# Optimization experiments

Hardware: AMD Instinct MI355X
Metric: run time of the kernel (lower is better)

Reference implementation:

```python
import jax, jax.numpy as jnp
import numpy as np

B, D, S, F, C, H, OUT = 4, 60, 512, 158, 64, 128, 1
LN_EPS = 1e-5


def setup_inputs() -> dict:
    key = jax.random.key(0)
    ks = jax.random.split(key, 12)
    g = lambda k, shape, s=0.05: jax.random.normal(k, shape, dtype=jnp.float32) * s
    return dict(
        x=jax.random.normal(ks[0], (B, D, S, F), dtype=jnp.float32),
        feature_mask=jax.random.randint(ks[1], (B, D, S), 0, 2).astype(bool),
        wq=g(ks[2], (F, C)), bq=jnp.zeros((C,), jnp.float32),
        wk=g(ks[3], (F, C)), bk=jnp.zeros((C,), jnp.float32),
        wv=g(ks[4], (F, C)), bv=jnp.zeros((C,), jnp.float32),
        ln_g=jnp.ones((F + C,), jnp.float32), ln_b=jnp.zeros((F + C,), jnp.float32),
        w_ih=g(ks[5], (3 * H, F + C)), w_hh=g(ks[6], (3 * H, H)),
        b_ih=jnp.zeros((3 * H,), jnp.float32), b_hh=jnp.zeros((3 * H,), jnp.float32),
        w1=g(ks[7], (H, H // 2)), b1=jnp.zeros((H // 2,), jnp.float32),
        w2=g(ks[8], (H // 2, OUT)), b2=jnp.zeros((OUT,), jnp.float32),
    )


def reference(x, feature_mask, wq, bq, wk, bk, wv, bv, ln_g, ln_b,
              w_ih, w_hh, b_ih, b_hh, w1, b1, w2, b2):
    b, d, s, f = x.shape
    c = wq.shape[1]
    h_dim = w_hh.shape[1]

    # --- market context attention, vectorized over (batch, days) ---
    Q = x @ wq + bq            # (B,D,S,C)
    K = x @ wk + bk
    V = x @ wv + bv
    scores = jnp.einsum('bdsc,bdtc->bdst', Q, K) / jnp.sqrt(jnp.float32(c))
    scores = jnp.where(feature_mask[:, :, None, :], scores, -1e9)  # mask keys
    attn = jax.nn.softmax(scores, axis=-1)
    ctx = jnp.einsum('bdst,bdtc->bdsc', attn, V)       # (B,D,S,C)
    ctx = jnp.where(feature_mask[..., None], ctx, 0.0)  # mask queries
    denom = jnp.maximum(feature_mask.sum(axis=2), 1).astype(x.dtype)  # (B,D)
    market = ctx.sum(axis=2) / denom[..., None]         # (B,D,C)

    # --- concat + layernorm ---
    aug = jnp.concatenate(
        [x, jnp.broadcast_to(market[:, :, None, :], (b, d, s, c))], axis=-1)
    mu = aug.mean(-1, keepdims=True)
    var = aug.var(-1, keepdims=True)
    aug = (aug - mu) / jnp.sqrt(var + LN_EPS) * ln_g + ln_b  # (B,D,S,F+C)

    # --- GRU over days, batch = B*S independent sequences ---
    seq = aug.transpose(1, 0, 2, 3).reshape(d, b * s, f + c)  # (D, N, F+C)
    x_proj = seq @ w_ih.T + b_ih                               # (D, N, 3H)

    def step(h, xp):
        hp = h @ w_hh.T + b_hh
        xr, xz, xn = jnp.split(xp, 3, axis=-1)
        hr, hz, hn = jnp.split(hp, 3, axis=-1)
        r = jax.nn.sigmoid(xr + hr)
        z = jax.nn.sigmoid(xz + hz)
        n = jnp.tanh(xn + r * hn)
        return (1.0 - z) * n + z * h, None

    h0 = jnp.zeros((b * s, h_dim), x.dtype)
    h_last, _ = jax.lax.scan(step, h0, x_proj)  # last-step output
    h_last = h_last.reshape(b, s, h_dim)

    # --- output head (dropout inactive in eval) ---
    hid = jax.nn.relu(h_last @ w1 + b1)
    return hid @ w2 + b2  # (B, S, OUT)
```

## Files before the change

kernel.cpp:

```cpp
#include <hip/hip_runtime.h>
#include <hip/hip_bf16.h>
#include <math.h>

#define BB 4
#define DD 60
#define SS 512
#define FF 158
#define CC 64
#define HH 128
#define FC 222
#define G3 384
#define NN 2048
#define BDN 240

typedef _Float16 f16x8 __attribute__((ext_vector_type(8)));
typedef float f32x4 __attribute__((ext_vector_type(4)));

__device__ __forceinline__ float sigmoidf_(float x){ return 1.0f/(1.0f+__expf(-x)); }
__device__ __forceinline__ float tanh_fast_(float x){
    float e = __expf(2.0f*x);
    return 1.0f - 2.0f/(e + 1.0f);
}

__global__ void prep_kernel(const float* __restrict__ w_ih,
                            const float* __restrict__ wq, const float* __restrict__ wk,
                            const float* __restrict__ wv, const float* __restrict__ w_hh,
                            _Float16* __restrict__ wf16, _Float16* __restrict__ wqkv,
                            _Float16* __restrict__ whh16){
    int idx = blockIdx.x*256 + threadIdx.x;
    if (idx < 384*224){
        int n = idx / 224, k = idx % 224;
        wf16[idx] = (k < FC) ? (_Float16)w_ih[n*FC + k] : (_Float16)0.0f;
    } else if (idx < 384*224 + 192*160){
        int i2 = idx - 384*224;
        int n = i2 / 160, k = i2 % 160;
        float v = 0.0f;
        if (k < FF){
            if (n < 64)       v = wq[k*CC + n];
            else if (n < 128) v = wk[k*CC + (n-64)];
            else              v = wv[k*CC + (n-128)];
        }
        wqkv[i2] = (_Float16)v;
    } else {
        int i3 = idx - (384*224 + 192*160);
        if (i3 < 384*128)
            whh16[i3] = (_Float16)w_hh[i3];
    }
}

__global__ __launch_bounds__(256) void qkv_kernel(const float* __restrict__ x,
                           const _Float16* __restrict__ wqkv,
                           const float* __restrict__ bq, const float* __restrict__ bk,
                           const float* __restrict__ bv,
                           _Float16* __restrict__ Qh, _Float16* __restrict__ Kh,
                           float* __restrict__ V){
    __shared__ _Float16 xa[5][64][40];
    int tid  = threadIdx.x;
    int lane = tid & 63, wv = tid >> 6;
    int col  = lane & 15, quad = lane >> 4;
    int row0 = blockIdx.x * 64;

    f16x8 bfr[3][5];
    #pragma unroll
    for (int nt = 0; nt < 3; ++nt){
        int n = wv*48 + nt*16 + col;
        #pragma unroll
        for (int kq = 0; kq < 5; ++kq)
            bfr[nt][kq] = *(const f16x8*)&wqkv[n*160 + kq*32 + quad*8];
    }

    for (int i = tid; i < 64*160; i += 256){
        int r = i / 160, k = i % 160;
        float v = (k < FF) ? x[(size_t)(row0 + r)*FF + k] : 0.0f;
        xa[k >> 5][r][k & 31] = (_Float16)v;
    }
    __syncthreads();

    float bias[3];
    #pragma unroll
    for (int nt = 0; nt < 3; ++nt){
        int n = wv*48 + nt*16 + col;
        bias[nt] = (n < 64) ? bq[n] : (n < 128 ? bk[n-64] : bv[n-128]);
    }

    #pragma unroll 1
    for (int mt = 0; mt < 4; ++mt){
        f16x8 a[5];
        #pragma unroll
        for (int kq = 0; kq < 5; ++kq)
            a[kq] = *(const f16x8*)&xa[kq][mt*16 + col][quad*8];
        #pragma unroll
        for (int nt = 0; nt < 3; ++nt){
            f32x4 c = {0.0f, 0.0f, 0.0f, 0.0f};
            #pragma unroll
            for (int kq = 0; kq < 5; ++kq)
                c = __builtin_amdgcn_mfma_f32_16x16x32_f16(a[kq], bfr[nt][kq], c, 0, 0, 0);
            int n = wv*48 + nt*16 + col;
            #pragma unroll
            for (int reg = 0; reg < 4; ++reg){
                int row = row0 + mt*16 + quad*4 + reg;
                float val = c[reg] + bias[nt];
                if (n < 64)       Qh[(size_t)row*CC + n]       = (_Float16)val;
                else if (n < 128) Kh[(size_t)row*CC + (n-64)]  = (_Float16)val;
                else              V [(size_t)row*CC + (n-128)] = val;
            }
        }
    }
}

__global__ __launch_bounds__(512) void attn_kernel(const _Float16* __restrict__ Qh,
                                                   const _Float16* __restrict__ Kh,
                                                   const int* __restrict__ mask,
                                                   const float* __restrict__ V,
                                                   float* __restrict__ market){
    __shared__ _Float16 kf[2][512][32];
    __shared__ float w_sh[512];
    __shared__ float mk_lds[512];

    int tid  = threadIdx.x;
    int bd   = blockIdx.x;
    int lane = tid & 63, wv = tid >> 6;
    int col  = lane & 15, quad = lane >> 4;

    const _Float16* qb = Qh + (size_t)(bd*SS)*CC;
    const _Float16* kb = Kh + (size_t)(bd*SS)*CC;

    {
        int t = tid;
        w_sh[t] = 0.0f;
        mk_lds[t] = (mask[bd*SS + t] != 0) ? 1.0f : 0.0f;
    }
    for (int i = tid; i < 4096; i += 512){
        int t = i >> 3, ch = i & 7;
        *(f16x8*)&kf[ch >> 2][t][(ch & 3)*8] = *(const f16x8*)&kb[t*CC + ch*8];
    }

    f16x8 a0[4], a1[4];
    #pragma unroll
    for (int af = 0; af < 4; ++af){
        int row = wv*64 + af*16 + col;
        a0[af] = *(const f16x8*)&qb[row*CC + quad*8];
        a1[af] = *(const f16x8*)&qb[row*CC + 32 + quad*8];
    }
    __syncthreads();

    float lacc[4][4] = {{0,0,0,0},{0,0,0,0},{0,0,0,0},{0,0,0,0}};
    #pragma unroll 2
    for (int kt = 0; kt < 32; ++kt){
        f16x8 b0 = *(const f16x8*)&kf[0][kt*16 + col][quad*8];
        f16x8 b1 = *(const f16x8*)&kf[1][kt*16 + col][quad*8];
        float mkv = mk_lds[kt*16 + col];
        #pragma unroll
        for (int af = 0; af < 4; ++af){
            f32x4 c = {0.0f, 0.0f, 0.0f, 0.0f};
            c = __builtin_amdgcn_mfma_f32_16x16x32_f16(a0[af], b0, c, 0, 0, 0);
            c = __builtin_amdgcn_mfma_f32_16x16x32_f16(a1[af], b1, c, 0, 0, 0);
            #pragma unroll
            for (int reg = 0; reg < 4; ++reg)
                lacc[af][reg] += __expf(c[reg]*0.125f) * mkv;
        }
    }
    float crv[4][4];
    #pragma unroll
    for (int af = 0; af < 4; ++af){
        #pragma unroll
        for (int reg = 0; reg < 4; ++reg){
            float l = lacc[af][reg];
            l += __shfl_xor(l, 1, 64);
            l += __shfl_xor(l, 2, 64);
            l += __shfl_xor(l, 4, 64);
            l += __shfl_xor(l, 8, 64);
            int row = wv*64 + af*16 + quad*4 + reg;
            crv[af][reg] = mk_lds[row] / l;
        }
    }

    #pragma unroll 2
    for (int kt = 0; kt < 32; ++kt){
        f16x8 b0 = *(const f16x8*)&kf[0][kt*16 + col][quad*8];
        f16x8 b1 = *(const f16x8*)&kf[1][kt*16 + col][quad*8];
        float s = 0.0f;
        #pragma unroll
        for (int af = 0; af < 4; ++af){
            f32x4 c = {0.0f, 0.0f, 0.0f, 0.0f};
            c = __builtin_amdgcn_mfma_f32_16x16x32_f16(a0[af], b0, c, 0, 0, 0);
            c = __builtin_amdgcn_mfma_f32_16x16x32_f16(a1[af], b1, c, 0, 0, 0);
            #pragma unroll
            for (int reg = 0; reg < 4; ++reg)
                s = fmaf(__expf(c[reg]*0.125f), crv[af][reg], s);
        }
        s += __shfl_xor(s, 16, 64);
        s += __shfl_xor(s, 32, 64);
        if (quad == 0)
            atomicAdd(&w_sh[kt*16 + col], s);
    }
    __syncthreads();

    float* msum = (float*)kf;
    {
        int c = tid & 63, grp = tid >> 6;
        const float* vb = V + (size_t)(bd*SS)*CC;
        float acc = 0.0f;
        int t0 = grp*64;
        #pragma unroll 4
        for (int t = t0; t < t0 + 64; ++t)
            acc = fmaf(w_sh[t]*mk_lds[t], vb[(size_t)t*CC + c], acc);
        msum[grp*64 + c] = acc;
    }
    __syncthreads();
    if (tid < 64){
        float s = 0.0f;
        #pragma unroll
        for (int g = 0; g < 8; ++g) s += msum[g*64 + tid];
        float cnt = 0.0f;
        #pragma unroll
        for (int j = 0; j < 8; ++j) cnt += mk_lds[tid + 64*j];
        #pragma unroll
        for (int o = 1; o < 64; o <<= 1) cnt += __shfl_xor(cnt, o, 64);
        market[bd*CC + tid] = s / fmaxf(cnt, 1.0f);
    }
}

__global__ __launch_bounds__(512, 2) void xproj_kernel(const float* __restrict__ x,
                             const float* __restrict__ market,
                             const float* __restrict__ ln_g, const float* __restrict__ ln_b,
                             const _Float16* __restrict__ wf16, const float* __restrict__ b_ih,
                             _Float16* __restrict__ XP){
    __shared__ _Float16 aug[7][64][32];
    int tid  = threadIdx.x;
    int lane = tid & 63, wv = tid >> 6;
    int col  = lane & 15, quad = lane >> 4;
    int row0 = blockIdx.x * 64;

    f16x8 bfr[3][7];
    #pragma unroll
    for (int nt = 0; nt < 3; ++nt){
        int n = wv*48 + nt*16 + col;
        #pragma unroll
        for (int kq = 0; kq < 7; ++kq)
            bfr[nt][kq] = *(const f16x8*)&wf16[n*224 + kq*32 + quad*8];
    }

    {
        int wrow = wv*8 + (lane >> 3);
        int g    = lane & 7;
        int row  = row0 + wrow;
        int d = row / NN, n = row % NN;
        int b = n >> 9, s = n & 511;
        const float* xr = &x[((size_t)((b*DD + d)*SS) + s)*FF];
        const float* mr = &market[(b*DD + d)*CC];
        float v[28];
        float sum = 0.0f, sq = 0.0f;
        #pragma unroll
        for (int j = 0; j < 28; ++j){
            int f = g + 8*j;
            float vv = 0.0f;
            if (f < FF) vv = xr[f];
            else if (f < FC) vv = mr[f - FF];
            v[j] = vv;
            sum += vv; sq += vv*vv;
        }
        sum += __shfl_xor(sum,1,64); sq += __shfl_xor(sq,1,64);
        sum += __shfl_xor(sum,2,64); sq += __shfl_xor(sq,2,64);
        sum += __shfl_xor(sum,4,64); sq += __shfl_xor(sq,4,64);
        float mu   = sum * (1.0f/222.0f);
        float var  = sq * (1.0f/222.0f) - mu*mu;
        float rstd = rsqrtf(var + 1e-5f);
        #pragma unroll
        for (int j = 0; j < 28; ++j){
            int f = g + 8*j;
            float val = (f < FC) ? ((v[j]-mu)*rstd*ln_g[f] + ln_b[f]) : 0.0f;
            aug[f>>5][wrow][f&31] = (_Float16)val;
        }
    }
    __syncthreads();

    float bias[3];
    #pragma unroll
    for (int nt = 0; nt < 3; ++nt) bias[nt] = b_ih[wv*48 + nt*16 + col];
    #pragma unroll 1
    for (int mt = 0; mt < 4; ++mt){
        f16x8 a[7];
        #pragma unroll
        for (int kq = 0; kq < 7; ++kq)
            a[kq] = *(const f16x8*)&aug[kq][mt*16 + col][quad*8];
        #pragma unroll
        for (int nt = 0; nt < 3; ++nt){
            f32x4 c = {0.0f, 0.0f, 0.0f, 0.0f};
            #pragma unroll
            for (int kq = 0; kq < 7; ++kq)
                c = __builtin_amdgcn_mfma_f32_16x16x32_f16(a[kq], bfr[nt][kq], c, 0, 0, 0);
            int nn = wv*48 + nt*16 + col;
            #pragma unroll
            for (int reg = 0; reg < 4; ++reg){
                int m = quad*4 + reg;
                XP[(size_t)(row0 + mt*16 + m)*G3 + nn] = (_Float16)(c[reg] + bias[nt]);
            }
        }
    }
}

#define XLOAD(dst, base_) do{                                                   \
    _Pragma("unroll") for (int rg_ = 0; rg_ < 4; ++rg_)                         \
    _Pragma("unroll") for (int g_ = 0; g_ < 3; ++g_)                            \
        dst[rg_][g_] = (base_)[rg_*G3 + g_*HH];                                 \
}while(0)

#define BARRIER_NODRAIN() asm volatile("s_waitcnt lgkmcnt(0)\ns_barrier" ::: "memory")

#define GRU_STEP(PRD, PWR, XC, XPF, DOPF) do{                                   \
    if (DOPF) { XLOAD(XPF, xp_d + 2*DSTR); }                                    \
    f16x8 a_[4];                                                                \
    _Pragma("unroll") for (int kq = 0; kq < 4; ++kq)                            \
        a_[kq] = *(const f16x8*)&hfrag[PRD][kq][col][quad*8];                   \
    f32x4 c0 = {0,0,0,0}, c1 = {0,0,0,0}, c2 = {0,0,0,0};                       \
    _Pragma("unroll") for (int kq = 0; kq < 4; ++kq)                            \
        c0 = __builtin_amdgcn_mfma_f32_16x16x32_f16(a_[kq], bfr[0][kq], c0, 0,0,0); \
    _Pragma("unroll") for (int kq = 0; kq < 4; ++kq)                            \
        c1 = __builtin_amdgcn_mfma_f32_16x16x32_f16(a_[kq], bfr[1][kq], c1, 0,0,0); \
    _Pragma("unroll") for (int kq = 0; kq < 4; ++kq)                            \
        c2 = __builtin_amdgcn_mfma_f32_16x16x32_f16(a_[kq], bfr[2][kq], c2, 0,0,0); \
    _Pragma("unroll") for (int rg = 0; rg < 4; ++rg){                           \
        float r_ = sigmoidf_((float)XC[rg][0] + c0[rg] + bh0);                  \
        float z_ = sigmoidf_((float)XC[rg][1] + c1[rg] + bh1);                  \
        float n_ = tanh_fast_((float)XC[rg][2] + r_*(c2[rg] + bh2));            \
        float h_ = n_ + z_*(hcur[rg] - n_);                                     \
        hcur[rg] = h_;                                                          \
        hfrag[PWR][w >> 1][quad*4 + rg][(w & 1)*16 + col] = (_Float16)h_;       \
    }                                                                           \
    xp_d += DSTR;                                                               \
    BARRIER_NODRAIN();                                                          \
}while(0)

__global__ __launch_bounds__(512) void gru_kernel(const _Float16* __restrict__ XP,
                                                  const _Float16* __restrict__ whh16,
                                                  const float* __restrict__ b_hh,
                                                  const float* __restrict__ w1, const float* __restrict__ b1,
                                                  const float* __restrict__ w2, const float* __restrict__ b2,
                                                  float* __restrict__ out){
    __shared__ _Float16 hfrag[2][4][16][40];
    __shared__ float h_sh[16][132];

    const int tid  = threadIdx.x;
    const int lane = tid & 63, w = tid >> 6;
    const int col  = lane & 15, quad = lane >> 4;
    const int row0 = blockIdx.x * 16;

    for (int i = tid; i < 2*4*16*40; i += 512)
        ((_Float16*)hfrag)[i] = (_Float16)0.0f;

    f16x8 bfr[3][4];
    #pragma unroll
    for (int g = 0; g < 3; ++g){
        #pragma unroll
        for (int kq = 0; kq < 4; ++kq)
            bfr[g][kq] = *(const f16x8*)&whh16[(size_t)(g*HH + w*16 + col)*HH + kq*32 + quad*8];
    }

    const float bh0 = b_hh[0*HH + w*16 + col];
    const float bh1 = b_hh[1*HH + w*16 + col];
    const float bh2 = b_hh[2*HH + w*16 + col];

    const size_t DSTR = (size_t)NN * G3;
    const _Float16* xp_d = XP + (size_t)(row0 + quad*4)*G3 + (w*16 + col);

    _Float16 xA[4][3], xB[4][3], xC[4][3];
    XLOAD(xA, xp_d);
    XLOAD(xB, xp_d + DSTR);

    float hcur[4] = {0.0f, 0.0f, 0.0f, 0.0f};
    __syncthreads();

    #pragma unroll 1
    for (int ch = 0; ch < 10; ++ch){
        const int pf = (ch < 9);
        GRU_STEP(0, 1, xA, xC, 1);
        GRU_STEP(1, 0, xB, xA, 1);
        GRU_STEP(0, 1, xC, xB, 1);
        GRU_STEP(1, 0, xA, xC, 1);
        GRU_STEP(0, 1, xB, xA, pf);
        GRU_STEP(1, 0, xC, xB, pf);
    }

    #pragma unroll
    for (int rg = 0; rg < 4; ++rg)
        h_sh[quad*4 + rg][w*16 + col] = hcur[rg];
    __syncthreads();

    {
        int c2 = tid & 63;
        int rb = tid >> 6;
        #pragma unroll
        for (int rr = 0; rr < 2; ++rr){
            int r = rb + rr*8;
            float acc = 0.0f;
            #pragma unroll 8
            for (int k = 0; k < 128; ++k)
                acc = fmaf(h_sh[r][k], w1[k*64 + c2], acc);
            float hid = fmaxf(acc + b1[c2], 0.0f);
            float o = hid * w2[c2];
            #pragma unroll
            for (int off = 1; off < 64; off <<= 1) o += __shfl_xor(o, off, 64);
            if (c2 == 0) out[row0 + r] = o + b2[0];
        }
    }
}

extern "C" void kernel_launch(void* const* d_in, const int* in_sizes, int n_in,
                              void* d_out, int out_size, void* d_ws, size_t ws_size,
                              hipStream_t stream) {
    const float* x    = (const float*)d_in[0];
    const int*   mask = (const int*)d_in[1];
    const float* wq   = (const float*)d_in[2];
    const float* bq   = (const float*)d_in[3];
    const float* wk   = (const float*)d_in[4];
    const float* bk   = (const float*)d_in[5];
    const float* wv   = (const float*)d_in[6];
    const float* bv   = (const float*)d_in[7];
    const float* ln_g = (const float*)d_in[8];
    const float* ln_b = (const float*)d_in[9];
    const float* w_ih = (const float*)d_in[10];
    const float* w_hh = (const float*)d_in[11];
    const float* b_ih = (const float*)d_in[12];
    const float* b_hh = (const float*)d_in[13];
    const float* w1   = (const float*)d_in[14];
    const float* b1   = (const float*)d_in[15];
    const float* w2   = (const float*)d_in[16];
    const float* b2   = (const float*)d_in[17];

    float* ws = (float*)d_ws;
    _Float16* Qh  = (_Float16*)ws;
    _Float16* Kh  = (_Float16*)(ws + 3932160);
    float*    V   = ws + 7864320;
    _Float16* XP  = (_Float16*)ws;
    float* market = ws + 23592960;
    _Float16* wf16 = (_Float16*)(ws + 23608320);
    _Float16* wqkv = (_Float16*)(ws + 23651328);
    _Float16* whh16= (_Float16*)(ws + 23666688);

    prep_kernel<<<648, 256, 0, stream>>>(w_ih, wq, wk, wv, w_hh, wf16, wqkv, whh16);
    qkv_kernel<<<1920, 256, 0, stream>>>(x, wqkv, bq, bk, bv, Qh, Kh, V);
    attn_kernel<<<240, 512, 0, stream>>>(Qh, Kh, mask, V, market);
    xproj_kernel<<<1920, 512, 0, stream>>>(x, market, ln_g, ln_b, wf16, b_ih, XP);
    gru_kernel<<<128, 512, 0, stream>>>(XP, whh16, b_hh, w1, b1, w2, b2, (float*)d_out);
}
```

Measured before the change: 375.9 us.

## Fold log2(e) into weights, use hardware exp2/rcp, halve GRU block warps

Pre-scales the GRU input and recurrent weights and biases by log2(e) (2·log2(e) for the candidate gate), and folds the attention 1/sqrt(C) and log2(e) factors into Q. This lets every exponential become a raw hardware exp2 and every division a hardware reciprocal, cutting transcendental cost in the attention softmax and the GRU gates. The GRU kernel also drops from 8 to 4 waves per block, with each wave covering 32 hidden columns in two halves, so it issues twice the MFMAs per wave and synchronises fewer waves at each step's barrier. Risks include a small precision loss from fp16 weight scaling and approximate rcp, and less latency hiding inside the serial recurrence.

```diff
diff --git a/kernel.cpp b/kernel.cpp
--- a/kernel.cpp
+++ b/kernel.cpp
@@ -13,14 +13,15 @@
 #define NN 2048
 #define BDN 240
 
+#define L2E  1.44269504f
+#define L2E2 2.88539008f
+#define QSCALE 0.18033688f
+
 typedef _Float16 f16x8 __attribute__((ext_vector_type(8)));
 typedef float f32x4 __attribute__((ext_vector_type(4)));
 
-__device__ __forceinline__ float sigmoidf_(float x){ return 1.0f/(1.0f+__expf(-x)); }
-__device__ __forceinline__ float tanh_fast_(float x){
-    float e = __expf(2.0f*x);
-    return 1.0f - 2.0f/(e + 1.0f);
-}
+__device__ __forceinline__ float exp2_hw(float x){ return __builtin_amdgcn_exp2f(x); }
+__device__ __forceinline__ float rcp_hw(float x){ return __builtin_amdgcn_rcpf(x); }
 
 __global__ void prep_kernel(const float* __restrict__ w_ih,
                             const float* __restrict__ wq, const float* __restrict__ wk,
@@ -30,7 +31,8 @@
     int idx = blockIdx.x*256 + threadIdx.x;
     if (idx < 384*224){
         int n = idx / 224, k = idx % 224;
-        wf16[idx] = (k < FC) ? (_Float16)w_ih[n*FC + k] : (_Float16)0.0f;
+        float sc = (n < 256) ? L2E : L2E2;
+        wf16[idx] = (k < FC) ? (_Float16)(w_ih[n*FC + k] * sc) : (_Float16)0.0f;
     } else if (idx < 384*224 + 192*160){
         int i2 = idx - 384*224;
         int n = i2 / 160, k = i2 % 160;
@@ -43,8 +45,11 @@
         wqkv[i2] = (_Float16)v;
     } else {
         int i3 = idx - (384*224 + 192*160);
-        if (i3 < 384*128)
-            whh16[i3] = (_Float16)w_hh[i3];
+        if (i3 < 384*128){
+            int n = i3 / 128;
+            float sc = (n < 256) ? L2E : L2E2;
+            whh16[i3] = (_Float16)(w_hh[i3] * sc);
+        }
     }
 }
 
@@ -100,7 +105,7 @@
             for (int reg = 0; reg < 4; ++reg){
                 int row = row0 + mt*16 + quad*4 + reg;
                 float val = c[reg] + bias[nt];
-                if (n < 64)       Qh[(size_t)row*CC + n]       = (_Float16)val;
+                if (n < 64)       Qh[(size_t)row*CC + n]       = (_Float16)(val * QSCALE);
                 else if (n < 128) Kh[(size_t)row*CC + (n-64)]  = (_Float16)val;
                 else              V [(size_t)row*CC + (n-128)] = val;
             }
@@ -157,7 +162,7 @@
             c = __builtin_amdgcn_mfma_f32_16x16x32_f16(a1[af], b1, c, 0, 0, 0);
             #pragma unroll
             for (int reg = 0; reg < 4; ++reg)
-                lacc[af][reg] += __expf(c[reg]*0.125f) * mkv;
+                lacc[af][reg] += exp2_hw(c[reg]) * mkv;
         }
     }
     float crv[4][4];
@@ -171,7 +176,7 @@
             l += __shfl_xor(l, 4, 64);
             l += __shfl_xor(l, 8, 64);
             int row = wv*64 + af*16 + quad*4 + reg;
-            crv[af][reg] = mk_lds[row] / l;
+            crv[af][reg] = mk_lds[row] * rcp_hw(l);
         }
     }
 
@@ -187,7 +192,7 @@
             c = __builtin_amdgcn_mfma_f32_16x16x32_f16(a1[af], b1, c, 0, 0, 0);
             #pragma unroll
             for (int reg = 0; reg < 4; ++reg)
-                s = fmaf(__expf(c[reg]*0.125f), crv[af][reg], s);
+                s = fmaf(exp2_hw(c[reg]), crv[af][reg], s);
         }
         s += __shfl_xor(s, 16, 64);
         s += __shfl_xor(s, 32, 64);
@@ -217,7 +222,7 @@
         for (int j = 0; j < 8; ++j) cnt += mk_lds[tid + 64*j];
         #pragma unroll
         for (int o = 1; o < 64; o <<= 1) cnt += __shfl_xor(cnt, o, 64);
-        market[bd*CC + tid] = s / fmaxf(cnt, 1.0f);
+        market[bd*CC + tid] = s * rcp_hw(fmaxf(cnt, 1.0f));
     }
 }
 
@@ -277,7 +282,10 @@
 
     float bias[3];
     #pragma unroll
-    for (int nt = 0; nt < 3; ++nt) bias[nt] = b_ih[wv*48 + nt*16 + col];
+    for (int nt = 0; nt < 3; ++nt){
+        int n = wv*48 + nt*16 + col;
+        bias[nt] = b_ih[n] * ((n < 256) ? L2E : L2E2);
+    }
     #pragma unroll 1
     for (int mt = 0; mt < 4; ++mt){
         f16x8 a[7];
@@ -301,9 +309,10 @@
 }
 
 #define XLOAD(dst, base_) do{                                                   \
+    _Pragma("unroll") for (int hf_ = 0; hf_ < 2; ++hf_)                         \
     _Pragma("unroll") for (int rg_ = 0; rg_ < 4; ++rg_)                         \
     _Pragma("unroll") for (int g_ = 0; g_ < 3; ++g_)                            \
-        dst[rg_][g_] = (base_)[rg_*G3 + g_*HH];                                 \
+        dst[hf_][rg_][g_] = (base_)[rg_*G3 + g_*HH + hf_*16];                   \
 }while(0)
 
 #define BARRIER_NODRAIN() asm volatile("s_waitcnt lgkmcnt(0)\ns_barrier" ::: "memory")
@@ -313,31 +322,34 @@
     f16x8 a_[4];                                                                \
     _Pragma("unroll") for (int kq = 0; kq < 4; ++kq)                            \
         a_[kq] = *(const f16x8*)&hfrag[PRD][kq][col][quad*8];                   \
-    f32x4 c0 = {0,0,0,0}, c1 = {0,0,0,0}, c2 = {0,0,0,0};                       \
-    _Pragma("unroll") for (int kq = 0; kq < 4; ++kq)                            \
-        c0 = __builtin_amdgcn_mfma_f32_16x16x32_f16(a_[kq], bfr[0][kq], c0, 0,0,0); \
-    _Pragma("unroll") for (int kq = 0; kq < 4; ++kq)                            \
-        c1 = __builtin_amdgcn_mfma_f32_16x16x32_f16(a_[kq], bfr[1][kq], c1, 0,0,0); \
-    _Pragma("unroll") for (int kq = 0; kq < 4; ++kq)                            \
-        c2 = __builtin_amdgcn_mfma_f32_16x16x32_f16(a_[kq], bfr[2][kq], c2, 0,0,0); \
+    f32x4 c_[3][2];                                                             \
+    _Pragma("unroll") for (int g = 0; g < 3; ++g)                               \
+    _Pragma("unroll") for (int hf = 0; hf < 2; ++hf){                           \
+        f32x4 acc = {0.0f, 0.0f, 0.0f, 0.0f};                                   \
+        _Pragma("unroll") for (int kq = 0; kq < 4; ++kq)                        \
+            acc = __builtin_amdgcn_mfma_f32_16x16x32_f16(a_[kq], bfr[g][hf][kq], acc, 0,0,0); \
+        c_[g][hf] = acc;                                                        \
+    }                                                                           \
+    _Pragma("unroll") for (int hf = 0; hf < 2; ++hf)                            \
     _Pragma("unroll") for (int rg = 0; rg < 4; ++rg){                           \
-        float r_ = sigmoidf_((float)XC[rg][0] + c0[rg] + bh0);                  \
-        float z_ = sigmoidf_((float)XC[rg][1] + c1[rg] + bh1);                  \
-        float n_ = tanh_fast_((float)XC[rg][2] + r_*(c2[rg] + bh2));            \
-        float h_ = n_ + z_*(hcur[rg] - n_);                                     \
-        hcur[rg] = h_;                                                          \
-        hfrag[PWR][w >> 1][quad*4 + rg][(w & 1)*16 + col] = (_Float16)h_;       \
+        float r_ = rcp_hw(1.0f + exp2_hw(-((float)XC[hf][rg][0] + c_[0][hf][rg] + bh[0][hf]))); \
+        float z_ = rcp_hw(1.0f + exp2_hw(-((float)XC[hf][rg][1] + c_[1][hf][rg] + bh[1][hf]))); \
+        float e_ = exp2_hw((float)XC[hf][rg][2] + r_*(c_[2][hf][rg] + bh[2][hf])); \
+        float n_ = 1.0f - 2.0f*rcp_hw(e_ + 1.0f);                               \
+        float h_ = n_ + z_*(hcur[hf][rg] - n_);                                 \
+        hcur[hf][rg] = h_;                                                      \
+        hfrag[PWR][w][quad*4 + rg][hf*16 + col] = (_Float16)h_;                 \
     }                                                                           \
     xp_d += DSTR;                                                               \
     BARRIER_NODRAIN();                                                          \
 }while(0)
 
-__global__ __launch_bounds__(512) void gru_kernel(const _Float16* __restrict__ XP,
-                                                  const _Float16* __restrict__ whh16,
-                                                  const float* __restrict__ b_hh,
-                                                  const float* __restrict__ w1, const float* __restrict__ b1,
-                                                  const float* __restrict__ w2, const float* __restrict__ b2,
-                                                  float* __restrict__ out){
+__global__ __launch_bounds__(256, 1) void gru_kernel(const _Float16* __restrict__ XP,
+                                                     const _Float16* __restrict__ whh16,
+                                                     const float* __restrict__ b_hh,
+                                                     const float* __restrict__ w1, const float* __restrict__ b1,
+                                                     const float* __restrict__ w2, const float* __restrict__ b2,
+                                                     float* __restrict__ out){
     __shared__ _Float16 hfrag[2][4][16][40];
     __shared__ float h_sh[16][132];
 
@@ -346,29 +358,35 @@
     const int col  = lane & 15, quad = lane >> 4;
     const int row0 = blockIdx.x * 16;
 
-    for (int i = tid; i < 2*4*16*40; i += 512)
+    for (int i = tid; i < 2*4*16*40; i += 256)
         ((_Float16*)hfrag)[i] = (_Float16)0.0f;
 
-    f16x8 bfr[3][4];
-    #pragma unroll
-    for (int g = 0; g < 3; ++g){
+    f16x8 bfr[3][2][4];
+    #pragma unroll
+    for (int g = 0; g < 3; ++g)
+    #pragma unroll
+    for (int hf = 0; hf < 2; ++hf){
+        int n = g*HH + w*32 + hf*16 + col;
         #pragma unroll
         for (int kq = 0; kq < 4; ++kq)
-            bfr[g][kq] = *(const f16x8*)&whh16[(size_t)(g*HH + w*16 + col)*HH + kq*32 + quad*8];
-    }
-
-    const float bh0 = b_hh[0*HH + w*16 + col];
-    const float bh1 = b_hh[1*HH + w*16 + col];
-    const float bh2 = b_hh[2*HH + w*16 + col];
+            bfr[g][hf][kq] = *(const f16x8*)&whh16[(size_t)n*HH + kq*32 + quad*8];
+    }
+
+    float bh[3][2];
+    #pragma unroll
+    for (int g = 0; g < 3; ++g)
+    #pragma unroll
+    for (int hf = 0; hf < 2; ++hf)
+        bh[g][hf] = b_hh[g*HH + w*32 + hf*16 + col] * ((g < 2) ? L2E : L2E2);
 
     const size_t DSTR = (size_t)NN * G3;
-    const _Float16* xp_d = XP + (size_t)(row0 + quad*4)*G3 + (w*16 + col);
-
-    _Float16 xA[4][3], xB[4][3], xC[4][3];
+    const _Float16* xp_d = XP + (size_t)(row0 + quad*4)*G3 + (w*32 + col);
+
+    _Float16 xA[2][4][3], xB[2][4][3], xC[2][4][3];
     XLOAD(xA, xp_d);
     XLOAD(xB, xp_d + DSTR);
 
-    float hcur[4] = {0.0f, 0.0f, 0.0f, 0.0f};
+    float hcur[2][4] = {{0,0,0,0},{0,0,0,0}};
     __syncthreads();
 
     #pragma unroll 1
@@ -383,16 +401,18 @@
     }
 
     #pragma unroll
+    for (int hf = 0; hf < 2; ++hf)
+    #pragma unroll
     for (int rg = 0; rg < 4; ++rg)
-        h_sh[quad*4 + rg][w*16 + col] = hcur[rg];
+        h_sh[quad*4 + rg][w*32 + hf*16 + col] = hcur[hf][rg];
     __syncthreads();
 
     {
         int c2 = tid & 63;
         int rb = tid >> 6;
         #pragma unroll
-        for (int rr = 0; rr < 2; ++rr){
-            int r = rb + rr*8;
+        for (int rr = 0; rr < 4; ++rr){
+            int r = rb*4 + rr;
             float acc = 0.0f;
             #pragma unroll 8
             for (int k = 0; k < 128; ++k)
@@ -442,5 +462,5 @@
     qkv_kernel<<<1920, 256, 0, stream>>>(x, wqkv, bq, bk, bv, Qh, Kh, V);
     attn_kernel<<<240, 512, 0, stream>>>(Qh, Kh, mask, V, market);
     xproj_kernel<<<1920, 512, 0, stream>>>(x, market, ln_g, ln_b, wf16, b_ih, XP);
-    gru_kernel<<<128, 512, 0, stream>>>(XP, whh16, b_hh, w1, b1, w2, b2, (float*)d_out);
-}
+    gru_kernel<<<128, 256, 0, stream>>>(XP, whh16, b_hh, w1, b1, w2, b2, (float*)d_out);
+}
```

Measured after the change: 356.8 us. 5.1% less time.
